# Optimization experiments

Measured on AMD Instinct MI355X. Metric: run time of the kernel, lower is better.

Reference implementation:

```python
import jax, jax.numpy as jnp
import numpy as np

PI = np.pi
WIN = (8, 8)
N = WIN[0] * WIN[1]          # 64 tokens per window
NUM_HEADS = 8
DIM = 256
HEAD_DIM = DIM // NUM_HEADS  # 32
P = 4                        # Fourier series order (hardcoded in module)
W_RES = 64                   # input_resolution[1]
SCALE = HEAD_DIM ** -0.5
B_ = 1024                    # num_windows * batch


def _azimuth():
    # relative_coords[:, :, 1] from the torch module: relative column offsets
    ch = np.arange(WIN[0])
    cw = np.arange(WIN[1])
    gh, gw = np.meshgrid(ch, cw, indexing='ij')
    cf = np.stack([gh.ravel(), gw.ravel()])          # (2, N)
    rel = cf[:, :, None] - cf[:, None, :]            # (2, N, N)
    return jnp.asarray(rel[1], dtype=jnp.float32)    # (N, N)


def setup_inputs() -> dict:
    key = jax.random.key(0)
    ks = jax.random.split(key, 12)
    std = 0.02
    return {
        'x': jax.random.normal(ks[0], (B_, N, DIM), dtype=jnp.float32),
        'D': jax.random.uniform(ks[1], (B_, N), dtype=jnp.float32),
        'a_p': std * jax.random.normal(ks[2], (P + 1, NUM_HEADS), dtype=jnp.float32),
        'b_p': std * jax.random.normal(ks[3], (P, NUM_HEADS), dtype=jnp.float32),
        'a_r': std * jax.random.normal(ks[4], (P + 1, NUM_HEADS), dtype=jnp.float32),
        'b_r': std * jax.random.normal(ks[5], (P, NUM_HEADS), dtype=jnp.float32),
        'qkv_w': std * jax.random.normal(ks[6], (3 * DIM, DIM), dtype=jnp.float32),
        'qkv_b': jnp.zeros((3 * DIM,), dtype=jnp.float32),
        'proj_w': std * jax.random.normal(ks[7], (DIM, DIM), dtype=jnp.float32),
        'proj_b': jnp.zeros((DIM,), dtype=jnp.float32),
    }


def reference(x, D, a_p, b_p, a_r, b_r, qkv_w, qkv_b, proj_w, proj_b):
    B, n, C = x.shape

    # ---- azimuth Fourier bias: A_phi, shape (H, N, N) ----
    az = _azimuth() * (2.0 * PI / W_RES)                       # (N, N)
    ii = jnp.arange(1, P + 1, dtype=x.dtype)[:, None, None]    # (P, 1, 1)
    cosP = jnp.cos(ii * az)                                    # (P, N, N)
    sinP = jnp.sin(ii * az)
    A_phi = (jnp.einsum('ph,pij->hij', a_p[1:], cosP)
             + jnp.einsum('ph,pij->hij', b_p, sinP)) / P + a_p[0][:, None, None]

    # ---- radius Fourier bias: A_r, shape (B, N, N, H); rad[b,i,j] = D[b,j] - D[b,i] ----
    rad = D[:, None, :] - D[:, :, None]                        # (B, N, N)
    r_max = 2.0                                                # module overwrites r_max = 2
    A_r = jnp.zeros(rad.shape + (NUM_HEADS,), dtype=x.dtype)
    for i in range(1, P + 1):
        arg = rad * (2.0 * PI * i / r_max)
        A_r = A_r + jnp.cos(arg)[..., None] * a_r[i] + jnp.sin(arg)[..., None] * b_r[i - 1]
    A_r = A_r / P + a_r[0]                                     # (B, N, N, H)

    # ---- attention ----
    qkv = (x @ qkv_w.T + qkv_b).reshape(B, n, 3, NUM_HEADS, HEAD_DIM)
    qkv = qkv.transpose(2, 0, 3, 1, 4)                         # (3, B, H, N, hd)
    q, k, v = qkv[0], qkv[1], qkv[2]
    attn = jnp.einsum('bhid,bhjd->bhij', q * SCALE, k)
    attn = attn + A_phi[None] + A_r.transpose(0, 3, 1, 2)
    attn = jax.nn.softmax(attn, axis=-1)
    out = jnp.einsum('bhij,bhjd->bhid', attn, v)
    out = out.transpose(0, 2, 1, 3).reshape(B, n, C)
    return out @ proj_w.T + proj_b
```

## Files before the change

kernel.cpp:

```cpp
#include <hip/hip_runtime.h>
#include <hip/hip_bf16.h>


using short8  = __attribute__((ext_vector_type(8))) short;
using short4v = __attribute__((ext_vector_type(4))) short;
using floatx4 = __attribute__((ext_vector_type(4))) float;

#define PI_F    3.14159265358979323846f
#define SCALE_F 0.17677669529663687f

__device__ __forceinline__ short bfs(float x) {
  __hip_bfloat16 h = __float2bfloat16(x);
  return __builtin_bit_cast(short, h);
}

__global__ void prep_kernel(const float* __restrict__ qw,
                            const float* __restrict__ pw,
                            __hip_bfloat16* __restrict__ dst) {
  int g = blockIdx.x * 256 + threadIdx.x;
  const float4* src;
  __hip_bfloat16* d;
  if (g < 49152) { src = (const float4*)qw + g; d = dst + g * 4; }
  else { int g2 = g - 49152; src = (const float4*)pw + g2; d = dst + 196608 + g2 * 4; }
  float4 v = *src;
  d[0] = __float2bfloat16(v.x);
  d[1] = __float2bfloat16(v.y);
  d[2] = __float2bfloat16(v.z);
  d[3] = __float2bfloat16(v.w);
}

__device__ __forceinline__ void fourier_feats(float dv, int col, float* f) {
  float s1, c1; __sincosf(PI_F * dv, &s1, &c1);
  float c2 = c1*c1 - s1*s1, s2 = 2.f*s1*c1;
  float c3 = c2*c1 - s2*s1, s3 = s2*c1 + c2*s1;
  float c4 = c2*c2 - s2*s2, s4 = 2.f*s2*c2;
  float sa1, ca1; __sincosf((2.f * PI_F / 64.f) * (float)col, &sa1, &ca1);
  float ca2 = ca1*ca1 - sa1*sa1, sa2 = 2.f*sa1*ca1;
  float ca3 = ca2*ca1 - sa2*sa1, sa3 = sa2*ca1 + ca2*sa1;
  float ca4 = ca2*ca2 - sa2*sa2, sa4 = 2.f*sa2*ca2;
  f[0]=c1;  f[1]=c2;  f[2]=c3;  f[3]=c4;
  f[4]=s1;  f[5]=s2;  f[6]=s3;  f[7]=s4;
  f[8]=ca1; f[9]=ca2; f[10]=ca3; f[11]=ca4;
  f[12]=sa1; f[13]=sa2; f[14]=sa3; f[15]=sa4;
}

__global__ __launch_bounds__(1024, 4) void fused_kernel(
    const float* __restrict__ x, const float* __restrict__ D,
    const float* __restrict__ a_p, const float* __restrict__ b_p,
    const float* __restrict__ a_r, const float* __restrict__ b_r,
    const __hip_bfloat16* __restrict__ wq, const float* __restrict__ qkv_b,
    const __hip_bfloat16* __restrict__ pwb, const float* __restrict__ pb,
    float* __restrict__ out)
{
  constexpr int LDX = 264, LDQ = 264, LDK = 264, LDQf = 40, LDKm = 136,
                LDVt = 72, LDP = 68, LDO = 264;
  __shared__ __align__(16) __hip_bfloat16 sScr[17408];
  __shared__ __align__(16) __hip_bfloat16 sQ  [64 * 264];
  __shared__ __align__(16) __hip_bfloat16 sK  [64 * 264];
  __shared__ __align__(16) __hip_bfloat16 sQf [64 * 40];
  __shared__ __align__(16) __hip_bfloat16 sKm [64 * 136];
  __shared__ __align__(16) __hip_bfloat16 sVt [256 * 72];

  const int tid = threadIdx.x;
  const int lane = tid & 63, w = tid >> 6;
  const int laneN = lane & 15, laneQ = lane >> 4;
  const int b = blockIdx.x;
  const floatx4 fzero = {0.f, 0.f, 0.f, 0.f};
  const short8 zero8 = {0, 0, 0, 0, 0, 0, 0, 0};

  const float4* xg = (const float4*)(x + (size_t)b * 16384);
  #pragma unroll
  for (int it = 0; it < 4; ++it) {
    int g = tid + it * 1024;
    float4 v = xg[g];
    int t = g >> 6, c = (g & 63) * 4;
    short4v pk = { bfs(v.x), bfs(v.y), bfs(v.z), bfs(v.w) };
    *(short4v*)&sScr[t * LDX + c] = pk;
  }
  if (tid < 64) {
    float f[16];
    fourier_feats(D[b * 64 + tid], tid & 7, f);
    short8 q0, q1;
    #pragma unroll
    for (int i = 0; i < 8; ++i) { q0[i] = bfs(f[i]); q1[i] = bfs(f[8 + i]); }
    *(short8*)&sQf[tid * LDQf +  0] = q0;
    *(short8*)&sQf[tid * LDQf +  8] = q1;
    *(short8*)&sQf[tid * LDQf + 16] = zero8;
    *(short8*)&sQf[tid * LDQf + 24] = zero8;
  }
  if (tid < 512) {
    int t = tid >> 3, hh = tid & 7;
    float f[16];
    fourier_feats(D[b * 64 + t], t & 7, f);
    short8 v0, v1;
    #pragma unroll
    for (int p = 0; p < 4; ++p) {
      float ar = a_r[(p + 1) * 8 + hh], br = b_r[p * 8 + hh];
      float ap = a_p[(p + 1) * 8 + hh], bp = b_p[p * 8 + hh];
      float cr = f[p], sr = f[4 + p], ca = f[8 + p], sa = f[12 + p];
      v0[p]     = bfs((ar * cr + br * sr) * 0.25f);
      v0[4 + p] = bfs((ar * sr - br * cr) * 0.25f);
      v1[p]     = bfs((ap * ca - bp * sa) * 0.25f);
      v1[4 + p] = bfs((ap * sa + bp * ca) * 0.25f);
    }
    *(short8*)&sKm[t * LDKm + hh * 16 + 0] = v0;
    *(short8*)&sKm[t * LDKm + hh * 16 + 8] = v1;
  }
  __syncthreads();

  {
    const __hip_bfloat16* w0 = wq + (size_t)(      w * 16 + laneN) * 256;
    const __hip_bfloat16* w1 = wq + (size_t)(256 + w * 16 + laneN) * 256;
    const __hip_bfloat16* w2 = wq + (size_t)(512 + w * 16 + laneN) * 256;
    floatx4 accQ[4], accK[4], accV[4];
    #pragma unroll
    for (int mt = 0; mt < 4; ++mt) { accQ[mt] = fzero; accK[mt] = fzero; accV[mt] = fzero; }
    #pragma unroll
    for (int kk = 0; kk < 8; ++kk) {
      short8 a4[4];
      #pragma unroll
      for (int mt = 0; mt < 4; ++mt)
        a4[mt] = *(const short8*)&sScr[(mt * 16 + laneN) * LDX + kk * 32 + laneQ * 8];
      short8 b0 = *(const short8*)&w0[kk * 32 + laneQ * 8];
      short8 b1 = *(const short8*)&w1[kk * 32 + laneQ * 8];
      short8 b2 = *(const short8*)&w2[kk * 32 + laneQ * 8];
      #pragma unroll
      for (int mt = 0; mt < 4; ++mt) {
        accQ[mt] = __builtin_amdgcn_mfma_f32_16x16x32_bf16(b0, a4[mt], accQ[mt], 0, 0, 0);
        accK[mt] = __builtin_amdgcn_mfma_f32_16x16x32_bf16(b1, a4[mt], accK[mt], 0, 0, 0);
        accV[mt] = __builtin_amdgcn_mfma_f32_16x16x32_bf16(a4[mt], b2, accV[mt], 0, 0, 0);
      }
    }
    float4 bq4 = *(const float4*)&qkv_b[      w * 16 + laneQ * 4];
    float4 bk4 = *(const float4*)&qkv_b[256 + w * 16 + laneQ * 4];
    float bv   = qkv_b[512 + w * 16 + laneN];
    float bqa[4] = {bq4.x, bq4.y, bq4.z, bq4.w};
    float bka[4] = {bk4.x, bk4.y, bk4.z, bk4.w};
    #pragma unroll
    for (int mt = 0; mt < 4; ++mt) {
      short4v pq, pk, pv;
      #pragma unroll
      for (int r = 0; r < 4; ++r) {
        pq[r] = bfs((accQ[mt][r] + bqa[r]) * SCALE_F);
        pk[r] = bfs(accK[mt][r] + bka[r]);
        pv[r] = bfs(accV[mt][r] + bv);
      }
      *(short4v*)&sQ [(mt * 16 + laneN) * LDQ + w * 16 + laneQ * 4] = pq;
      *(short4v*)&sK [(mt * 16 + laneN) * LDK + w * 16 + laneQ * 4] = pk;
      *(short4v*)&sVt[(w * 16 + laneN) * LDVt + mt * 16 + laneQ * 4] = pv;
    }
  }
  __syncthreads();

  const int h = w >> 1, gm0 = (w & 1) * 2;
  short8 kf0[4], kf1[4];
  #pragma unroll
  for (int nt = 0; nt < 4; ++nt) {
    kf0[nt] = *(const short8*)&sK[(nt * 16 + laneN) * LDK + h * 32 + laneQ * 8];
    short8 km = *(const short8*)&sKm[(nt * 16 + laneN) * LDKm + h * 16 + (laneQ & 1) * 8];
    kf1[nt] = (laneQ < 2) ? km : zero8;
  }
  short8 vb[2][2];
  #pragma unroll
  for (int ont = 0; ont < 2; ++ont)
    #pragma unroll
    for (int kk = 0; kk < 2; ++kk)
      vb[ont][kk] = *(const short8*)&sVt[(h * 32 + ont * 16 + laneN) * LDVt + kk * 32 + laneQ * 8];

  floatx4 oacc[2][2];
  __hip_bfloat16* Pw = &sScr[w * 16 * LDP];
  #pragma unroll
  for (int m = 0; m < 2; ++m) {
    const int gm = gm0 + m;
    short8 q0 = *(const short8*)&sQ [(gm * 16 + laneN) * LDQ + h * 32 + laneQ * 8];
    short8 q1 = *(const short8*)&sQf[(gm * 16 + laneN) * LDQf + laneQ * 8];
    floatx4 s[4];
    #pragma unroll
    for (int nt = 0; nt < 4; ++nt) {
      s[nt] = __builtin_amdgcn_mfma_f32_16x16x32_bf16(q0, kf0[nt], fzero, 0, 0, 0);
      s[nt] = __builtin_amdgcn_mfma_f32_16x16x32_bf16(q1, kf1[nt], s[nt], 0, 0, 0);
    }
    #pragma unroll
    for (int r = 0; r < 4; ++r) {
      float mx = fmaxf(fmaxf(s[0][r], s[1][r]), fmaxf(s[2][r], s[3][r]));
      mx = fmaxf(mx, __shfl_xor(mx, 1));
      mx = fmaxf(mx, __shfl_xor(mx, 2));
      mx = fmaxf(mx, __shfl_xor(mx, 4));
      mx = fmaxf(mx, __shfl_xor(mx, 8));
      float e0 = __expf(s[0][r] - mx), e1 = __expf(s[1][r] - mx);
      float e2 = __expf(s[2][r] - mx), e3 = __expf(s[3][r] - mx);
      float sum = e0 + e1 + e2 + e3;
      sum += __shfl_xor(sum, 1);
      sum += __shfl_xor(sum, 2);
      sum += __shfl_xor(sum, 4);
      sum += __shfl_xor(sum, 8);
      float inv = __builtin_amdgcn_rcpf(sum);
      int pr = laneQ * 4 + r;
      Pw[pr * LDP +  0 + laneN] = __float2bfloat16(e0 * inv);
      Pw[pr * LDP + 16 + laneN] = __float2bfloat16(e1 * inv);
      Pw[pr * LDP + 32 + laneN] = __float2bfloat16(e2 * inv);
      Pw[pr * LDP + 48 + laneN] = __float2bfloat16(e3 * inv);
    }
    short4v p0a = *(const short4v*)&Pw[laneN * LDP + laneQ * 8];
    short4v p0b = *(const short4v*)&Pw[laneN * LDP + laneQ * 8 + 4];
    short4v p1a = *(const short4v*)&Pw[laneN * LDP + 32 + laneQ * 8];
    short4v p1b = *(const short4v*)&Pw[laneN * LDP + 36 + laneQ * 8];
    short8 pf0 = __builtin_shufflevector(p0a, p0b, 0, 1, 2, 3, 4, 5, 6, 7);
    short8 pf1 = __builtin_shufflevector(p1a, p1b, 0, 1, 2, 3, 4, 5, 6, 7);
    #pragma unroll
    for (int ont = 0; ont < 2; ++ont) {
      oacc[m][ont] = __builtin_amdgcn_mfma_f32_16x16x32_bf16(vb[ont][0], pf0, fzero, 0, 0, 0);
      oacc[m][ont] = __builtin_amdgcn_mfma_f32_16x16x32_bf16(vb[ont][1], pf1, oacc[m][ont], 0, 0, 0);
    }
  }
  __syncthreads();

  #pragma unroll
  for (int m = 0; m < 2; ++m)
    #pragma unroll
    for (int ont = 0; ont < 2; ++ont) {
      short4v pk;
      #pragma unroll
      for (int r = 0; r < 4; ++r) pk[r] = bfs(oacc[m][ont][r]);
      *(short4v*)&sScr[((gm0 + m) * 16 + laneN) * LDO + h * 32 + ont * 16 + laneQ * 4] = pk;
    }
  __syncthreads();

  const int col0 = w * 16;
  floatx4 pacc[4] = {fzero, fzero, fzero, fzero};
  const __hip_bfloat16* prow = pwb + (size_t)(col0 + laneN) * 256;
  #pragma unroll
  for (int kk = 0; kk < 8; ++kk) {
    short8 pbf = *(const short8*)&prow[kk * 32 + laneQ * 8];
    #pragma unroll
    for (int mt = 0; mt < 4; ++mt) {
      short8 pa = *(const short8*)&sScr[(mt * 16 + laneN) * LDO + kk * 32 + laneQ * 8];
      pacc[mt] = __builtin_amdgcn_mfma_f32_16x16x32_bf16(pbf, pa, pacc[mt], 0, 0, 0);
    }
  }
  float4 bias4 = *(const float4*)&pb[col0 + laneQ * 4];
  float* og = out + (size_t)b * 16384;
  #pragma unroll
  for (int mt = 0; mt < 4; ++mt) {
    float4 o4;
    o4.x = pacc[mt][0] + bias4.x;
    o4.y = pacc[mt][1] + bias4.y;
    o4.z = pacc[mt][2] + bias4.z;
    o4.w = pacc[mt][3] + bias4.w;
    *(float4*)&og[(mt * 16 + laneN) * 256 + col0 + laneQ * 4] = o4;
  }
}

extern "C" void kernel_launch(void* const* d_in, const int* in_sizes, int n_in,
                              void* d_out, int out_size, void* d_ws, size_t ws_size,
                              hipStream_t stream) {
  const float* x      = (const float*)d_in[0];
  const float* D      = (const float*)d_in[1];
  const float* a_p    = (const float*)d_in[2];
  const float* b_p    = (const float*)d_in[3];
  const float* a_r    = (const float*)d_in[4];
  const float* b_r    = (const float*)d_in[5];
  const float* qkv_w  = (const float*)d_in[6];
  const float* qkv_b  = (const float*)d_in[7];
  const float* proj_w = (const float*)d_in[8];
  const float* proj_b = (const float*)d_in[9];

  __hip_bfloat16* wq  = (__hip_bfloat16*)d_ws;
  __hip_bfloat16* pwb = wq + 196608;
  float* out = (float*)d_out;

  prep_kernel<<<256, 256, 0, stream>>>(qkv_w, proj_w, wq);
  fused_kernel<<<1024, 1024, 0, stream>>>(x, D, a_p, b_p, a_r, b_r, wq, qkv_b,
                                          pwb, proj_b, out);
}
```

Baseline: 215.2 us.

## Split fused attention kernel into QKV projection and attention kernels via workspace

Splits the single large fused kernel into a QKV projection kernel that writes bf16 Q, K and transposed V to global workspace, and an attention-plus-projection kernel that reads them back. Both use 512-thread blocks with much smaller shared-memory footprints, so more blocks can be resident per CU. The cost is an extra global round trip of about 96 MB of bf16 intermediates. The old fused path is kept as a fallback when the workspace is too small.

Measured after the change: 611.5 us. 2.84x slower.

```diff
diff --git a/kernel.cpp b/kernel.cpp
--- a/kernel.cpp
+++ b/kernel.cpp
@@ -44,39 +44,123 @@
   f[12]=sa1; f[13]=sa2; f[14]=sa3; f[15]=sa4;
 }
 
-__global__ __launch_bounds__(1024, 4) void fused_kernel(
-    const float* __restrict__ x, const float* __restrict__ D,
-    const float* __restrict__ a_p, const float* __restrict__ b_p,
-    const float* __restrict__ a_r, const float* __restrict__ b_r,
+__global__ __launch_bounds__(512, 8) void qkv_kernel(
+    const float* __restrict__ x,
     const __hip_bfloat16* __restrict__ wq, const float* __restrict__ qkv_b,
-    const __hip_bfloat16* __restrict__ pwb, const float* __restrict__ pb,
-    float* __restrict__ out)
+    __hip_bfloat16* __restrict__ Qg, __hip_bfloat16* __restrict__ Kg,
+    __hip_bfloat16* __restrict__ Vtg)
 {
-  constexpr int LDX = 264, LDQ = 264, LDK = 264, LDQf = 40, LDKm = 136,
-                LDVt = 72, LDP = 68, LDO = 264;
-  __shared__ __align__(16) __hip_bfloat16 sScr[17408];
-  __shared__ __align__(16) __hip_bfloat16 sQ  [64 * 264];
-  __shared__ __align__(16) __hip_bfloat16 sK  [64 * 264];
-  __shared__ __align__(16) __hip_bfloat16 sQf [64 * 40];
-  __shared__ __align__(16) __hip_bfloat16 sKm [64 * 136];
-  __shared__ __align__(16) __hip_bfloat16 sVt [256 * 72];
+  constexpr int LDX = 264;
+  __shared__ __align__(16) __hip_bfloat16 sX[64 * LDX];
 
   const int tid = threadIdx.x;
   const int lane = tid & 63, w = tid >> 6;
   const int laneN = lane & 15, laneQ = lane >> 4;
   const int b = blockIdx.x;
   const floatx4 fzero = {0.f, 0.f, 0.f, 0.f};
-  const short8 zero8 = {0, 0, 0, 0, 0, 0, 0, 0};
 
   const float4* xg = (const float4*)(x + (size_t)b * 16384);
   #pragma unroll
-  for (int it = 0; it < 4; ++it) {
-    int g = tid + it * 1024;
+  for (int it = 0; it < 8; ++it) {
+    int g = tid + it * 512;
     float4 v = xg[g];
     int t = g >> 6, c = (g & 63) * 4;
     short4v pk = { bfs(v.x), bfs(v.y), bfs(v.z), bfs(v.w) };
-    *(short4v*)&sScr[t * LDX + c] = pk;
-  }
+    *(short4v*)&sX[t * LDX + c] = pk;
+  }
+  __syncthreads();
+
+  floatx4 acc[6][4];
+  #pragma unroll
+  for (int ni = 0; ni < 6; ++ni)
+    #pragma unroll
+    for (int mt = 0; mt < 4; ++mt) acc[ni][mt] = fzero;
+
+  #pragma unroll
+  for (int kk = 0; kk < 8; ++kk) {
+    short8 a4[4];
+    #pragma unroll
+    for (int mt = 0; mt < 4; ++mt)
+      a4[mt] = *(const short8*)&sX[(mt * 16 + laneN) * LDX + kk * 32 + laneQ * 8];
+    #pragma unroll
+    for (int ni = 0; ni < 6; ++ni) {
+      int wrow = w * 16 + ni * 128 + laneN;
+      short8 bf = *(const short8*)&wq[(size_t)wrow * 256 + kk * 32 + laneQ * 8];
+      if (ni < 4) {
+        #pragma unroll
+        for (int mt = 0; mt < 4; ++mt)
+          acc[ni][mt] = __builtin_amdgcn_mfma_f32_16x16x32_bf16(bf, a4[mt], acc[ni][mt], 0, 0, 0);
+      } else {
+        #pragma unroll
+        for (int mt = 0; mt < 4; ++mt)
+          acc[ni][mt] = __builtin_amdgcn_mfma_f32_16x16x32_bf16(a4[mt], bf, acc[ni][mt], 0, 0, 0);
+      }
+    }
+  }
+
+  const size_t base = (size_t)b * 16384;
+  #pragma unroll
+  for (int ni = 0; ni < 2; ++ni) {
+    int qc = w * 16 + ni * 128;
+    float4 b4 = *(const float4*)&qkv_b[qc + laneQ * 4];
+    float ba[4] = {b4.x, b4.y, b4.z, b4.w};
+    #pragma unroll
+    for (int mt = 0; mt < 4; ++mt) {
+      short4v pq;
+      #pragma unroll
+      for (int r = 0; r < 4; ++r) pq[r] = bfs((acc[ni][mt][r] + ba[r]) * SCALE_F);
+      *(short4v*)&Qg[base + (mt * 16 + laneN) * 256 + qc + laneQ * 4] = pq;
+    }
+  }
+  #pragma unroll
+  for (int ni = 2; ni < 4; ++ni) {
+    int kc = w * 16 + (ni - 2) * 128;
+    float4 b4 = *(const float4*)&qkv_b[256 + kc + laneQ * 4];
+    float ba[4] = {b4.x, b4.y, b4.z, b4.w};
+    #pragma unroll
+    for (int mt = 0; mt < 4; ++mt) {
+      short4v pk;
+      #pragma unroll
+      for (int r = 0; r < 4; ++r) pk[r] = bfs(acc[ni][mt][r] + ba[r]);
+      *(short4v*)&Kg[base + (mt * 16 + laneN) * 256 + kc + laneQ * 4] = pk;
+    }
+  }
+  #pragma unroll
+  for (int ni = 4; ni < 6; ++ni) {
+    int vc = w * 16 + (ni - 4) * 128;
+    float bv = qkv_b[512 + vc + laneN];
+    #pragma unroll
+    for (int mt = 0; mt < 4; ++mt) {
+      short4v pv;
+      #pragma unroll
+      for (int r = 0; r < 4; ++r) pv[r] = bfs(acc[ni][mt][r] + bv);
+      *(short4v*)&Vtg[base + (vc + laneN) * 64 + mt * 16 + laneQ * 4] = pv;
+    }
+  }
+}
+
+__global__ __launch_bounds__(512, 4) void attn_kernel(
+    const float* __restrict__ D,
+    const float* __restrict__ a_p, const float* __restrict__ b_p,
+    const float* __restrict__ a_r, const float* __restrict__ b_r,
+    const __hip_bfloat16* __restrict__ Qg, const __hip_bfloat16* __restrict__ Kg,
+    const __hip_bfloat16* __restrict__ Vtg,
+    const __hip_bfloat16* __restrict__ pwb, const float* __restrict__ pb,
+    float* __restrict__ out)
+{
+  constexpr int LDO = 264, LDP = 68, LDQf = 40, LDKm = 136;
+  __shared__ __align__(16) __hip_bfloat16 sO [64 * LDO];
+  __shared__ __align__(16) __hip_bfloat16 sQf[64 * LDQf];
+  __shared__ __align__(16) __hip_bfloat16 sKm[64 * LDKm];
+
+  const int tid = threadIdx.x;
+  const int lane = tid & 63, w = tid >> 6;
+  const int laneN = lane & 15, laneQ = lane >> 4;
+  const int b = blockIdx.x;
+  const size_t base = (size_t)b * 16384;
+  const floatx4 fzero = {0.f, 0.f, 0.f, 0.f};
+  const short8 zero8 = {0, 0, 0, 0, 0, 0, 0, 0};
+
   if (tid < 64) {
     float f[16];
     fourier_feats(D[b * 64 + tid], tid & 7, f);
@@ -88,7 +172,7 @@
     *(short8*)&sQf[tid * LDQf + 16] = zero8;
     *(short8*)&sQf[tid * LDQf + 24] = zero8;
   }
-  if (tid < 512) {
+  {
     int t = tid >> 3, hh = tid & 7;
     float f[16];
     fourier_feats(D[b * 64 + t], t & 7, f);
@@ -108,55 +192,11 @@
   }
   __syncthreads();
 
-  {
-    const __hip_bfloat16* w0 = wq + (size_t)(      w * 16 + laneN) * 256;
-    const __hip_bfloat16* w1 = wq + (size_t)(256 + w * 16 + laneN) * 256;
-    const __hip_bfloat16* w2 = wq + (size_t)(512 + w * 16 + laneN) * 256;
-    floatx4 accQ[4], accK[4], accV[4];
-    #pragma unroll
-    for (int mt = 0; mt < 4; ++mt) { accQ[mt] = fzero; accK[mt] = fzero; accV[mt] = fzero; }
-    #pragma unroll
-    for (int kk = 0; kk < 8; ++kk) {
-      short8 a4[4];
-      #pragma unroll
-      for (int mt = 0; mt < 4; ++mt)
-        a4[mt] = *(const short8*)&sScr[(mt * 16 + laneN) * LDX + kk * 32 + laneQ * 8];
-      short8 b0 = *(const short8*)&w0[kk * 32 + laneQ * 8];
-      short8 b1 = *(const short8*)&w1[kk * 32 + laneQ * 8];
-      short8 b2 = *(const short8*)&w2[kk * 32 + laneQ * 8];
-      #pragma unroll
-      for (int mt = 0; mt < 4; ++mt) {
-        accQ[mt] = __builtin_amdgcn_mfma_f32_16x16x32_bf16(b0, a4[mt], accQ[mt], 0, 0, 0);
-        accK[mt] = __builtin_amdgcn_mfma_f32_16x16x32_bf16(b1, a4[mt], accK[mt], 0, 0, 0);
-        accV[mt] = __builtin_amdgcn_mfma_f32_16x16x32_bf16(a4[mt], b2, accV[mt], 0, 0, 0);
-      }
-    }
-    float4 bq4 = *(const float4*)&qkv_b[      w * 16 + laneQ * 4];
-    float4 bk4 = *(const float4*)&qkv_b[256 + w * 16 + laneQ * 4];
-    float bv   = qkv_b[512 + w * 16 + laneN];
-    float bqa[4] = {bq4.x, bq4.y, bq4.z, bq4.w};
-    float bka[4] = {bk4.x, bk4.y, bk4.z, bk4.w};
-    #pragma unroll
-    for (int mt = 0; mt < 4; ++mt) {
-      short4v pq, pk, pv;
-      #pragma unroll
-      for (int r = 0; r < 4; ++r) {
-        pq[r] = bfs((accQ[mt][r] + bqa[r]) * SCALE_F);
-        pk[r] = bfs(accK[mt][r] + bka[r]);
-        pv[r] = bfs(accV[mt][r] + bv);
-      }
-      *(short4v*)&sQ [(mt * 16 + laneN) * LDQ + w * 16 + laneQ * 4] = pq;
-      *(short4v*)&sK [(mt * 16 + laneN) * LDK + w * 16 + laneQ * 4] = pk;
-      *(short4v*)&sVt[(w * 16 + laneN) * LDVt + mt * 16 + laneQ * 4] = pv;
-    }
-  }
-  __syncthreads();
-
-  const int h = w >> 1, gm0 = (w & 1) * 2;
+  const int h = w;
   short8 kf0[4], kf1[4];
   #pragma unroll
   for (int nt = 0; nt < 4; ++nt) {
-    kf0[nt] = *(const short8*)&sK[(nt * 16 + laneN) * LDK + h * 32 + laneQ * 8];
+    kf0[nt] = *(const short8*)&Kg[base + (nt * 16 + laneN) * 256 + h * 32 + laneQ * 8];
     short8 km = *(const short8*)&sKm[(nt * 16 + laneN) * LDKm + h * 16 + (laneQ & 1) * 8];
     kf1[nt] = (laneQ < 2) ? km : zero8;
   }
@@ -165,15 +205,14 @@
   for (int ont = 0; ont < 2; ++ont)
     #pragma unroll
     for (int kk = 0; kk < 2; ++kk)
-      vb[ont][kk] = *(const short8*)&sVt[(h * 32 + ont * 16 + laneN) * LDVt + kk * 32 + laneQ * 8];
-
-  floatx4 oacc[2][2];
-  __hip_bfloat16* Pw = &sScr[w * 16 * LDP];
-  #pragma unroll
-  for (int m = 0; m < 2; ++m) {
-    const int gm = gm0 + m;
-    short8 q0 = *(const short8*)&sQ [(gm * 16 + laneN) * LDQ + h * 32 + laneQ * 8];
-    short8 q1 = *(const short8*)&sQf[(gm * 16 + laneN) * LDQf + laneQ * 8];
+      vb[ont][kk] = *(const short8*)&Vtg[base + (h * 32 + ont * 16 + laneN) * 64 + kk * 32 + laneQ * 8];
+
+  floatx4 oacc[4][2];
+  __hip_bfloat16* Pw = &sO[w * 16 * LDP];
+  #pragma unroll
+  for (int mt = 0; mt < 4; ++mt) {
+    short8 q0 = *(const short8*)&Qg[base + (mt * 16 + laneN) * 256 + h * 32 + laneQ * 8];
+    short8 q1 = *(const short8*)&sQf[(mt * 16 + laneN) * LDQf + laneQ * 8];
     floatx4 s[4];
     #pragma unroll
     for (int nt = 0; nt < 4; ++nt) {
@@ -209,6 +248,223 @@
     short8 pf1 = __builtin_shufflevector(p1a, p1b, 0, 1, 2, 3, 4, 5, 6, 7);
     #pragma unroll
     for (int ont = 0; ont < 2; ++ont) {
+      oacc[mt][ont] = __builtin_amdgcn_mfma_f32_16x16x32_bf16(vb[ont][0], pf0, fzero, 0, 0, 0);
+      oacc[mt][ont] = __builtin_amdgcn_mfma_f32_16x16x32_bf16(vb[ont][1], pf1, oacc[mt][ont], 0, 0, 0);
+    }
+  }
+  __syncthreads();
+
+  #pragma unroll
+  for (int mt = 0; mt < 4; ++mt)
+    #pragma unroll
+    for (int ont = 0; ont < 2; ++ont) {
+      short4v pk;
+      #pragma unroll
+      for (int r = 0; r < 4; ++r) pk[r] = bfs(oacc[mt][ont][r]);
+      *(short4v*)&sO[(mt * 16 + laneN) * LDO + h * 32 + ont * 16 + laneQ * 4] = pk;
+    }
+  __syncthreads();
+
+  floatx4 pacc[4][2];
+  #pragma unroll
+  for (int mt = 0; mt < 4; ++mt) { pacc[mt][0] = fzero; pacc[mt][1] = fzero; }
+  #pragma unroll
+  for (int kk = 0; kk < 8; ++kk) {
+    short8 pa[4], pbf[2];
+    #pragma unroll
+    for (int mt = 0; mt < 4; ++mt)
+      pa[mt] = *(const short8*)&sO[(mt * 16 + laneN) * LDO + kk * 32 + laneQ * 8];
+    #pragma unroll
+    for (int n2 = 0; n2 < 2; ++n2)
+      pbf[n2] = *(const short8*)&pwb[(size_t)(w * 32 + n2 * 16 + laneN) * 256 + kk * 32 + laneQ * 8];
+    #pragma unroll
+    for (int mt = 0; mt < 4; ++mt)
+      #pragma unroll
+      for (int n2 = 0; n2 < 2; ++n2)
+        pacc[mt][n2] = __builtin_amdgcn_mfma_f32_16x16x32_bf16(pbf[n2], pa[mt], pacc[mt][n2], 0, 0, 0);
+  }
+  float* og = out + (size_t)b * 16384;
+  #pragma unroll
+  for (int n2 = 0; n2 < 2; ++n2) {
+    int col0 = w * 32 + n2 * 16;
+    float4 bias4 = *(const float4*)&pb[col0 + laneQ * 4];
+    #pragma unroll
+    for (int mt = 0; mt < 4; ++mt) {
+      float4 o4;
+      o4.x = pacc[mt][n2][0] + bias4.x;
+      o4.y = pacc[mt][n2][1] + bias4.y;
+      o4.z = pacc[mt][n2][2] + bias4.z;
+      o4.w = pacc[mt][n2][3] + bias4.w;
+      *(float4*)&og[(mt * 16 + laneN) * 256 + col0 + laneQ * 4] = o4;
+    }
+  }
+}
+
+__global__ __launch_bounds__(1024, 4) void fused_kernel(
+    const float* __restrict__ x, const float* __restrict__ D,
+    const float* __restrict__ a_p, const float* __restrict__ b_p,
+    const float* __restrict__ a_r, const float* __restrict__ b_r,
+    const __hip_bfloat16* __restrict__ wq, const float* __restrict__ qkv_b,
+    const __hip_bfloat16* __restrict__ pwb, const float* __restrict__ pb,
+    float* __restrict__ out)
+{
+  constexpr int LDX = 264, LDQ = 264, LDK = 264, LDQf = 40, LDKm = 136,
+                LDVt = 72, LDP = 68, LDO = 264;
+  __shared__ __align__(16) __hip_bfloat16 sScr[17408];
+  __shared__ __align__(16) __hip_bfloat16 sQ  [64 * 264];
+  __shared__ __align__(16) __hip_bfloat16 sK  [64 * 264];
+  __shared__ __align__(16) __hip_bfloat16 sQf [64 * 40];
+  __shared__ __align__(16) __hip_bfloat16 sKm [64 * 136];
+  __shared__ __align__(16) __hip_bfloat16 sVt [256 * 72];
+
+  const int tid = threadIdx.x;
+  const int lane = tid & 63, w = tid >> 6;
+  const int laneN = lane & 15, laneQ = lane >> 4;
+  const int b = blockIdx.x;
+  const floatx4 fzero = {0.f, 0.f, 0.f, 0.f};
+  const short8 zero8 = {0, 0, 0, 0, 0, 0, 0, 0};
+
+  const float4* xg = (const float4*)(x + (size_t)b * 16384);
+  #pragma unroll
+  for (int it = 0; it < 4; ++it) {
+    int g = tid + it * 1024;
+    float4 v = xg[g];
+    int t = g >> 6, c = (g & 63) * 4;
+    short4v pk = { bfs(v.x), bfs(v.y), bfs(v.z), bfs(v.w) };
+    *(short4v*)&sScr[t * LDX + c] = pk;
+  }
+  if (tid < 64) {
+    float f[16];
+    fourier_feats(D[b * 64 + tid], tid & 7, f);
+    short8 q0, q1;
+    #pragma unroll
+    for (int i = 0; i < 8; ++i) { q0[i] = bfs(f[i]); q1[i] = bfs(f[8 + i]); }
+    *(short8*)&sQf[tid * LDQf +  0] = q0;
+    *(short8*)&sQf[tid * LDQf +  8] = q1;
+    *(short8*)&sQf[tid * LDQf + 16] = zero8;
+    *(short8*)&sQf[tid * LDQf + 24] = zero8;
+  }
+  if (tid < 512) {
+    int t = tid >> 3, hh = tid & 7;
+    float f[16];
+    fourier_feats(D[b * 64 + t], t & 7, f);
+    short8 v0, v1;
+    #pragma unroll
+    for (int p = 0; p < 4; ++p) {
+      float ar = a_r[(p + 1) * 8 + hh], br = b_r[p * 8 + hh];
+      float ap = a_p[(p + 1) * 8 + hh], bp = b_p[p * 8 + hh];
+      float cr = f[p], sr = f[4 + p], ca = f[8 + p], sa = f[12 + p];
+      v0[p]     = bfs((ar * cr + br * sr) * 0.25f);
+      v0[4 + p] = bfs((ar * sr - br * cr) * 0.25f);
+      v1[p]     = bfs((ap * ca - bp * sa) * 0.25f);
+      v1[4 + p] = bfs((ap * sa + bp * ca) * 0.25f);
+    }
+    *(short8*)&sKm[t * LDKm + hh * 16 + 0] = v0;
+    *(short8*)&sKm[t * LDKm + hh * 16 + 8] = v1;
+  }
+  __syncthreads();
+
+  {
+    const __hip_bfloat16* w0 = wq + (size_t)(      w * 16 + laneN) * 256;
+    const __hip_bfloat16* w1 = wq + (size_t)(256 + w * 16 + laneN) * 256;
+    const __hip_bfloat16* w2 = wq + (size_t)(512 + w * 16 + laneN) * 256;
+    floatx4 accQ[4], accK[4], accV[4];
+    #pragma unroll
+    for (int mt = 0; mt < 4; ++mt) { accQ[mt] = fzero; accK[mt] = fzero; accV[mt] = fzero; }
+    #pragma unroll
+    for (int kk = 0; kk < 8; ++kk) {
+      short8 a4[4];
+      #pragma unroll
+      for (int mt = 0; mt < 4; ++mt)
+        a4[mt] = *(const short8*)&sScr[(mt * 16 + laneN) * LDX + kk * 32 + laneQ * 8];
+      short8 b0 = *(const short8*)&w0[kk * 32 + laneQ * 8];
+      short8 b1 = *(const short8*)&w1[kk * 32 + laneQ * 8];
+      short8 b2 = *(const short8*)&w2[kk * 32 + laneQ * 8];
+      #pragma unroll
+      for (int mt = 0; mt < 4; ++mt) {
+        accQ[mt] = __builtin_amdgcn_mfma_f32_16x16x32_bf16(b0, a4[mt], accQ[mt], 0, 0, 0);
+        accK[mt] = __builtin_amdgcn_mfma_f32_16x16x32_bf16(b1, a4[mt], accK[mt], 0, 0, 0);
+        accV[mt] = __builtin_amdgcn_mfma_f32_16x16x32_bf16(a4[mt], b2, accV[mt], 0, 0, 0);
+      }
+    }
+    float4 bq4 = *(const float4*)&qkv_b[      w * 16 + laneQ * 4];
+    float4 bk4 = *(const float4*)&qkv_b[256 + w * 16 + laneQ * 4];
+    float bv   = qkv_b[512 + w * 16 + laneN];
+    float bqa[4] = {bq4.x, bq4.y, bq4.z, bq4.w};
+    float bka[4] = {bk4.x, bk4.y, bk4.z, bk4.w};
+    #pragma unroll
+    for (int mt = 0; mt < 4; ++mt) {
+      short4v pq, pk, pv;
+      #pragma unroll
+      for (int r = 0; r < 4; ++r) {
+        pq[r] = bfs((accQ[mt][r] + bqa[r]) * SCALE_F);
+        pk[r] = bfs(accK[mt][r] + bka[r]);
+        pv[r] = bfs(accV[mt][r] + bv);
+      }
+      *(short4v*)&sQ [(mt * 16 + laneN) * LDQ + w * 16 + laneQ * 4] = pq;
+      *(short4v*)&sK [(mt * 16 + laneN) * LDK + w * 16 + laneQ * 4] = pk;
+      *(short4v*)&sVt[(w * 16 + laneN) * LDVt + mt * 16 + laneQ * 4] = pv;
+    }
+  }
+  __syncthreads();
+
+  const int h = w >> 1, gm0 = (w & 1) * 2;
+  short8 kf0[4], kf1[4];
+  #pragma unroll
+  for (int nt = 0; nt < 4; ++nt) {
+    kf0[nt] = *(const short8*)&sK[(nt * 16 + laneN) * LDK + h * 32 + laneQ * 8];
+    short8 km = *(const short8*)&sKm[(nt * 16 + laneN) * LDKm + h * 16 + (laneQ & 1) * 8];
+    kf1[nt] = (laneQ < 2) ? km : zero8;
+  }
+  short8 vb[2][2];
+  #pragma unroll
+  for (int ont = 0; ont < 2; ++ont)
+    #pragma unroll
+    for (int kk = 0; kk < 2; ++kk)
+      vb[ont][kk] = *(const short8*)&sVt[(h * 32 + ont * 16 + laneN) * LDVt + kk * 32 + laneQ * 8];
+
+  floatx4 oacc[2][2];
+  __hip_bfloat16* Pw = &sScr[w * 16 * LDP];
+  #pragma unroll
+  for (int m = 0; m < 2; ++m) {
+    const int gm = gm0 + m;
+    short8 q0 = *(const short8*)&sQ [(gm * 16 + laneN) * LDQ + h * 32 + laneQ * 8];
+    short8 q1 = *(const short8*)&sQf[(gm * 16 + laneN) * LDQf + laneQ * 8];
+    floatx4 s[4];
+    #pragma unroll
+    for (int nt = 0; nt < 4; ++nt) {
+      s[nt] = __builtin_amdgcn_mfma_f32_16x16x32_bf16(q0, kf0[nt], fzero, 0, 0, 0);
+      s[nt] = __builtin_amdgcn_mfma_f32_16x16x32_bf16(q1, kf1[nt], s[nt], 0, 0, 0);
+    }
+    #pragma unroll
+    for (int r = 0; r < 4; ++r) {
+      float mx = fmaxf(fmaxf(s[0][r], s[1][r]), fmaxf(s[2][r], s[3][r]));
+      mx = fmaxf(mx, __shfl_xor(mx, 1));
+      mx = fmaxf(mx, __shfl_xor(mx, 2));
+      mx = fmaxf(mx, __shfl_xor(mx, 4));
+      mx = fmaxf(mx, __shfl_xor(mx, 8));
+      float e0 = __expf(s[0][r] - mx), e1 = __expf(s[1][r] - mx);
+      float e2 = __expf(s[2][r] - mx), e3 = __expf(s[3][r] - mx);
+      float sum = e0 + e1 + e2 + e3;
+      sum += __shfl_xor(sum, 1);
+      sum += __shfl_xor(sum, 2);
+      sum += __shfl_xor(sum, 4);
+      sum += __shfl_xor(sum, 8);
+      float inv = __builtin_amdgcn_rcpf(sum);
+      int pr = laneQ * 4 + r;
+      Pw[pr * LDP +  0 + laneN] = __float2bfloat16(e0 * inv);
+      Pw[pr * LDP + 16 + laneN] = __float2bfloat16(e1 * inv);
+      Pw[pr * LDP + 32 + laneN] = __float2bfloat16(e2 * inv);
+      Pw[pr * LDP + 48 + laneN] = __float2bfloat16(e3 * inv);
+    }
+    short4v p0a = *(const short4v*)&Pw[laneN * LDP + laneQ * 8];
+    short4v p0b = *(const short4v*)&Pw[laneN * LDP + laneQ * 8 + 4];
+    short4v p1a = *(const short4v*)&Pw[laneN * LDP + 32 + laneQ * 8];
+    short4v p1b = *(const short4v*)&Pw[laneN * LDP + 36 + laneQ * 8];
+    short8 pf0 = __builtin_shufflevector(p0a, p0b, 0, 1, 2, 3, 4, 5, 6, 7);
+    short8 pf1 = __builtin_shufflevector(p1a, p1b, 0, 1, 2, 3, 4, 5, 6, 7);
+    #pragma unroll
+    for (int ont = 0; ont < 2; ++ont) {
       oacc[m][ont] = __builtin_amdgcn_mfma_f32_16x16x32_bf16(vb[ont][0], pf0, fzero, 0, 0, 0);
       oacc[m][ont] = __builtin_amdgcn_mfma_f32_16x16x32_bf16(vb[ont][1], pf1, oacc[m][ont], 0, 0, 0);
     }
@@ -270,6 +526,20 @@
   float* out = (float*)d_out;
 
   prep_kernel<<<256, 256, 0, stream>>>(qkv_w, proj_w, wq);
-  fused_kernel<<<1024, 1024, 0, stream>>>(x, D, a_p, b_p, a_r, b_r, wq, qkv_b,
+
+  const size_t WEIGHT_BYTES = 524288;
+  const size_t QKV_ELEMS    = (size_t)1024 * 16384;
+  const size_t NEED = WEIGHT_BYTES + 3 * QKV_ELEMS * 2;
+
+  if (ws_size >= NEED) {
+    __hip_bfloat16* Qg  = (__hip_bfloat16*)((char*)d_ws + WEIGHT_BYTES);
+    __hip_bfloat16* Kg  = Qg + QKV_ELEMS;
+    __hip_bfloat16* Vtg = Kg + QKV_ELEMS;
+    qkv_kernel<<<1024, 512, 0, stream>>>(x, wq, qkv_b, Qg, Kg, Vtg);
+    attn_kernel<<<1024, 512, 0, stream>>>(D, a_p, b_p, a_r, b_r, Qg, Kg, Vtg,
                                           pwb, proj_b, out);
-}
+  } else {
+    fused_kernel<<<1024, 1024, 0, stream>>>(x, D, a_p, b_p, a_r, b_r, wq, qkv_b,
+                                            pwb, proj_b, out);
+  }
+}
```
